# Optimization experiments

Measured on AMD Instinct MI355X. Metric: run time of the kernel, lower is better.

## Reference

```python
import jax, jax.numpy as jnp
from jax import lax
import numpy as np


def setup_inputs() -> dict:
    key = jax.random.key(0)
    kb, ks = jax.random.split(key)
    boxes = jax.random.uniform(kb, (4, 2048, 4), dtype=jnp.float32)
    scores = jax.random.normal(ks, (4, 16, 2048), dtype=jnp.float32)
    return {
        "boxes": boxes,
        "scores": scores,
        "max_output_boxes_per_class": 100,
        "iou_threshold": jnp.float32(0.5),
        "score_threshold": jnp.float32(0.0),
    }


def _fix_boxes(boxes):
    # center_point_box == 0 path: reorder corners so x1<=x2, y1<=y2
    # (swap-if-greater in the original is equivalent to per-axis min/max)
    x1, y1, x2, y2 = boxes[..., 0], boxes[..., 1], boxes[..., 2], boxes[..., 3]
    return jnp.stack(
        [jnp.minimum(x1, x2), jnp.minimum(y1, y2), jnp.maximum(x1, x2), jnp.maximum(y1, y2)],
        axis=-1,
    )


def _nms_single(boxes, scores, iou_thr, score_thr, K):
    # boxes: [N,4] (xyxy, already fixed), scores: [N]
    N = boxes.shape[0]
    order = jnp.argsort(-scores)  # stable sort -> ties broken by index, like torchvision
    b = boxes[order]
    x1, y1, x2, y2 = b[:, 0], b[:, 1], b[:, 2], b[:, 3]
    area = (x2 - x1) * (y2 - y1)
    idxs = jnp.arange(N)

    def step(suppressed, k):
        kept = ~suppressed[k]
        ix1 = jnp.maximum(b[k, 0], x1)
        iy1 = jnp.maximum(b[k, 1], y1)
        ix2 = jnp.minimum(b[k, 2], x2)
        iy2 = jnp.minimum(b[k, 3], y2)
        inter = jnp.maximum(ix2 - ix1, 0.0) * jnp.maximum(iy2 - iy1, 0.0)
        iou = inter / (area[k] + area - inter)
        suppressed = suppressed | (kept & (iou > iou_thr) & (idxs > k))
        return suppressed, kept

    _, keep = lax.scan(step, jnp.zeros((N,), bool), idxs)  # keep: [N] in score order
    rank = jnp.cumsum(keep) - 1
    slot = jnp.where(keep & (rank < K), rank, K)  # slot K is out-of-bounds -> dropped
    sel = jnp.full((K,), -1, jnp.int32).at[slot].set(order.astype(jnp.int32), mode="drop")
    # original truncates the top-K selection to the COUNT of selected boxes passing score_thr
    sel_valid = sel >= 0
    count = jnp.sum(sel_valid & (scores[jnp.maximum(sel, 0)] >= score_thr))
    return jnp.where(jnp.arange(K) < count, sel, -1)


def reference(boxes, scores, max_output_boxes_per_class, iou_threshold, score_threshold):
    B, N, _ = boxes.shape
    C = scores.shape[1]
    K = int(max_output_boxes_per_class)
    fb = _fix_boxes(boxes)
    f = lambda bx, sc: _nms_single(bx, sc, iou_threshold, score_threshold, K)
    # vmap over classes (boxes shared), then over batch
    sel = jax.vmap(jax.vmap(f, in_axes=(None, 0)), in_axes=(0, 0))(fb, scores)  # [B,C,K]
    valid = sel >= 0
    bidx = jnp.broadcast_to(jnp.arange(B, dtype=jnp.int32)[:, None, None], sel.shape)
    cidx = jnp.broadcast_to(jnp.arange(C, dtype=jnp.int32)[None, :, None], sel.shape)
    out = jnp.stack([jnp.where(valid, bidx, -1), jnp.where(valid, cidx, -1), sel], axis=-1)
    # fixed-shape padded version of the original ragged [num_selected, 3] output;
    # invalid rows are all -1
    return out.reshape(B * C * K, 3)
```

## Files before the change

kernel.cpp:

```cpp
#include <hip/hip_runtime.h>

#define NN 2048
#define NT 256
#define NB 4
#define NC 16
#define NCLS (NB * NC)
#define CHUNKS 8
#define TILE 64
#define NTILES (NN / TILE)
#define KKEEP 176

typedef unsigned long long u64;

__device__ __forceinline__ u64 make_key(float s, int idx) {
  unsigned u = __float_as_uint(s);
  u ^= (u >> 31) ? 0xFFFFFFFFu : 0x80000000u;
  u = ~u;
  return ((u64)u << 32) | (unsigned)idx;
}
__device__ __forceinline__ float key_score(u64 key) {
  unsigned u = ~(unsigned)(key >> 32);
  unsigned bits = (u >> 31) ? (u ^ 0x80000000u) : ~u;
  return __uint_as_float(bits);
}

__device__ __forceinline__ float iou_f(float kx1, float ky1, float kx2, float ky2, float ka,
                                       float x1, float y1, float x2, float y2, float a) {
  float ix1 = fmaxf(kx1, x1);
  float iy1 = fmaxf(ky1, y1);
  float ix2 = fminf(kx2, x2);
  float iy2 = fminf(ky2, y2);
  float iw = fmaxf(ix2 - ix1, 0.0f);
  float ih = fmaxf(iy2 - iy1, 0.0f);
  float inter = iw * ih;
  asm volatile("" : "+v"(inter));
  float denom = ka + a - inter;
  return inter / denom;
}

__global__ __launch_bounds__(NT) void rank_kernel(
    const float* __restrict__ boxes,
    const float* __restrict__ scores,
    float* __restrict__ wx1, float* __restrict__ wy1,
    float* __restrict__ wx2, float* __restrict__ wy2,
    float* __restrict__ wsc, int* __restrict__ widx)
{
  __shared__ u64 s_key[NN];

  const int blk   = blockIdx.x;
  const int bc    = blk >> 3;
  const int chunk = blk & 7;
  const int b     = bc >> 4;
  const int t     = threadIdx.x;

  {
    const float4* s4 = (const float4*)(scores + (size_t)bc * NN);
    float4 v0 = s4[t * 2], v1 = s4[t * 2 + 1];
    const int g = t * 8;
    s_key[g + 0] = make_key(v0.x, g + 0);
    s_key[g + 1] = make_key(v0.y, g + 1);
    s_key[g + 2] = make_key(v0.z, g + 2);
    s_key[g + 3] = make_key(v0.w, g + 3);
    s_key[g + 4] = make_key(v1.x, g + 4);
    s_key[g + 5] = make_key(v1.y, g + 5);
    s_key[g + 6] = make_key(v1.z, g + 6);
    s_key[g + 7] = make_key(v1.w, g + 7);
  }
  __syncthreads();

  const int i = chunk * NT + t;
  const u64 my = s_key[i];

  int r0 = 0, r1 = 0, r2 = 0, r3 = 0;
#pragma unroll 4
  for (int j = 0; j < NN; j += 4) {
    r0 += (s_key[j + 0] < my) ? 1 : 0;
    r1 += (s_key[j + 1] < my) ? 1 : 0;
    r2 += (s_key[j + 2] < my) ? 1 : 0;
    r3 += (s_key[j + 3] < my) ? 1 : 0;
  }
  const int rank = r0 + r1 + r2 + r3;

  const int idx = (int)(unsigned)(my & 0xFFFFFFFFu);
  float4 v = *(const float4*)(boxes + ((size_t)b * NN + idx) * 4);
  float x1 = fminf(v.x, v.z), x2 = fmaxf(v.x, v.z);
  float y1 = fminf(v.y, v.w), y2 = fmaxf(v.y, v.w);

  const size_t o = (size_t)bc * NN + rank;
  wx1[o] = x1; wy1[o] = y1;
  wx2[o] = x2; wy2[o] = y2;
  wsc[o] = key_score(my);
  widx[o] = idx;
}

__global__ __launch_bounds__(NT) void greedy_kernel(
    const float* __restrict__ wx1, const float* __restrict__ wy1,
    const float* __restrict__ wx2, const float* __restrict__ wy2,
    const float* __restrict__ wsc, const int* __restrict__ widx,
    const float* __restrict__ iou_thr_p, const float* __restrict__ score_thr_p,
    int K, int* __restrict__ out)
{
  __shared__ float s_kx1[KKEEP], s_ky1[KKEEP], s_kx2[KKEEP], s_ky2[KKEEP], s_ka[KKEEP];
  __shared__ float s_tx1[TILE], s_ty1[TILE], s_tx2[TILE], s_ty2[TILE], s_ts[TILE];
  __shared__ int   s_tidx[TILE];
  __shared__ u64   s_colmask[4][TILE];
  __shared__ u64   s_dead[4];
  __shared__ int   s_total;

  const int bc = blockIdx.x;
  const int b  = bc >> 4;
  const int c  = bc & 15;
  const int t  = threadIdx.x;
  const int wv = t >> 6;
  const int ln = t & 63;

  const float iou_thr = *iou_thr_p;
  const float sthr    = *score_thr_p;

  int* orow = out + (size_t)bc * K * 3;
  for (int i = t; i < K * 3; i += NT) orow[i] = -1;
  if (t == 0) s_total = 0;

  const size_t base0 = (size_t)bc * NN;
  __syncthreads();

  for (int tile = 0; tile < NTILES; tile++) {
    const int base = tile * TILE;

    if      (wv == 0) { s_tx1[ln] = wx1[base0 + base + ln]; s_ts[ln]   = wsc[base0 + base + ln]; }
    else if (wv == 1) { s_ty1[ln] = wy1[base0 + base + ln]; s_tidx[ln] = widx[base0 + base + ln]; }
    else if (wv == 2) { s_tx2[ln] = wx2[base0 + base + ln]; }
    else              { s_ty2[ln] = wy2[base0 + base + ln]; }
    const int kcount = s_total;
    __syncthreads();

    float jx1 = s_tx1[ln], jy1 = s_ty1[ln], jx2 = s_tx2[ln], jy2 = s_ty2[ln];
    float ja  = (jx2 - jx1) * (jy2 - jy1);
    u64 m = 0ULL;
    for (int r = 0; r < 16; r++) {
      int il = wv * 16 + r;
      if (il < ln) {
        float rx1 = s_tx1[il], ry1 = s_ty1[il], rx2 = s_tx2[il], ry2 = s_ty2[il];
        float ra  = (rx2 - rx1) * (ry2 - ry1);
        float iou = iou_f(rx1, ry1, rx2, ry2, ra, jx1, jy1, jx2, jy2, ja);
        if (iou > iou_thr) m |= (1ULL << il);
      }
    }
    s_colmask[wv][ln] = m;

    bool dead = false;
    for (int ki = wv; ki < kcount; ki += 4) {
      float iou = iou_f(s_kx1[ki], s_ky1[ki], s_kx2[ki], s_ky2[ki], s_ka[ki],
                        jx1, jy1, jx2, jy2, ja);
      if (iou > iou_thr) { dead = true; break; }
    }
    s_dead[wv] = __ballot(dead);
    __syncthreads();

    if (t < 64) {
      u64 mc = s_colmask[0][ln] | s_colmask[1][ln] | s_colmask[2][ln] | s_colmask[3][ln];
      u64 alive = ~(s_dead[0] | s_dead[1] | s_dead[2] | s_dead[3]);
      for (int i = 0; i < TILE; i++) {
        if ((alive >> i) & 1ULL) {
          u64 kill = __ballot((int)((mc >> i) & 1ULL));
          alive &= ~kill;
        }
      }
      int total0 = s_total;
      bool kept = (alive >> ln) & 1ULL;
      int pos = __popcll(alive & ((1ULL << ln) - 1ULL));
      if (kept) {
        int kpos = total0 + pos;
        s_kx1[kpos] = jx1; s_ky1[kpos] = jy1;
        s_kx2[kpos] = jx2; s_ky2[kpos] = jy2; s_ka[kpos] = ja;
        if (kpos < K && s_ts[ln] >= sthr) {
          orow[kpos * 3 + 0] = b;
          orow[kpos * 3 + 1] = c;
          orow[kpos * 3 + 2] = s_tidx[ln];
        }
      }
      if (ln == 0) s_total = total0 + (int)__popcll(alive);
    }
    __syncthreads();
    if (s_total >= K) break;
  }
}

extern "C" void kernel_launch(void* const* d_in, const int* in_sizes, int n_in,
                              void* d_out, int out_size, void* d_ws, size_t ws_size,
                              hipStream_t stream) {
  const float* boxes  = (const float*)d_in[0];
  const float* scores = (const float*)d_in[1];
  const float* iou_p  = (const float*)d_in[3];
  const float* sth_p  = (const float*)d_in[4];
  int* out = (int*)d_out;

  const int K = out_size / (NCLS * 3);
  const size_t plane = (size_t)NCLS * NN;

  float* w   = (float*)d_ws;
  float* wx1 = w + 0 * plane;
  float* wy1 = w + 1 * plane;
  float* wx2 = w + 2 * plane;
  float* wy2 = w + 3 * plane;
  float* wsc = w + 4 * plane;
  int*  widx = (int*)(w + 5 * plane);

  hipLaunchKernelGGL(rank_kernel, dim3(NCLS * CHUNKS), dim3(NT), 0, stream,
                     boxes, scores, wx1, wy1, wx2, wy2, wsc, widx);
  hipLaunchKernelGGL(greedy_kernel, dim3(NCLS), dim3(NT), 0, stream,
                     wx1, wy1, wx2, wy2, wsc, widx, iou_p, sth_p, K, out);
}
```

Before: 53.17 us.

## Precompute sort keys in separate kernel and rank from global memory

Adds a key_kernel that writes the 64-bit score/index keys once per class to workspace. The rank kernel then reads keys straight from global memory (wave-uniform broadcast loads through the cache) instead of building a 16KB LDS copy in every block, and the rank loop is unrolled to 8 accumulators. This removes the redundant per-chunk key construction and the LDS barrier, but adds a kernel launch and swaps LDS reads for scalar or global loads whose latency may be higher.

```diff
diff --git a/kernel.cpp b/kernel.cpp
--- a/kernel.cpp
+++ b/kernel.cpp
@@ -38,48 +38,54 @@
   return inter / denom;
 }
 
+__global__ __launch_bounds__(NT) void key_kernel(
+    const float* __restrict__ scores, u64* __restrict__ keys)
+{
+  const int bc = blockIdx.x;
+  const int t  = threadIdx.x;
+  const float4* s4 = (const float4*)(scores + (size_t)bc * NN);
+  float4 v0 = s4[t * 2], v1 = s4[t * 2 + 1];
+  const int g = t * 8;
+  u64* kp = keys + (size_t)bc * NN + g;
+  kp[0] = make_key(v0.x, g + 0);
+  kp[1] = make_key(v0.y, g + 1);
+  kp[2] = make_key(v0.z, g + 2);
+  kp[3] = make_key(v0.w, g + 3);
+  kp[4] = make_key(v1.x, g + 4);
+  kp[5] = make_key(v1.y, g + 5);
+  kp[6] = make_key(v1.z, g + 6);
+  kp[7] = make_key(v1.w, g + 7);
+}
+
 __global__ __launch_bounds__(NT) void rank_kernel(
+    const u64* __restrict__ keys,
     const float* __restrict__ boxes,
-    const float* __restrict__ scores,
     float* __restrict__ wx1, float* __restrict__ wy1,
     float* __restrict__ wx2, float* __restrict__ wy2,
     float* __restrict__ wsc, int* __restrict__ widx)
 {
-  __shared__ u64 s_key[NN];
-
   const int blk   = blockIdx.x;
   const int bc    = blk >> 3;
   const int chunk = blk & 7;
   const int b     = bc >> 4;
   const int t     = threadIdx.x;
 
-  {
-    const float4* s4 = (const float4*)(scores + (size_t)bc * NN);
-    float4 v0 = s4[t * 2], v1 = s4[t * 2 + 1];
-    const int g = t * 8;
-    s_key[g + 0] = make_key(v0.x, g + 0);
-    s_key[g + 1] = make_key(v0.y, g + 1);
-    s_key[g + 2] = make_key(v0.z, g + 2);
-    s_key[g + 3] = make_key(v0.w, g + 3);
-    s_key[g + 4] = make_key(v1.x, g + 4);
-    s_key[g + 5] = make_key(v1.y, g + 5);
-    s_key[g + 6] = make_key(v1.z, g + 6);
-    s_key[g + 7] = make_key(v1.w, g + 7);
+  const u64* __restrict__ kcls = keys + (size_t)bc * NN;
+  const int i = chunk * NT + t;
+  const u64 my = kcls[i];
+
+  int r0 = 0, r1 = 0, r2 = 0, r3 = 0, r4 = 0, r5 = 0, r6 = 0, r7 = 0;
+  for (int j = 0; j < NN; j += 8) {
+    r0 += (kcls[j + 0] < my) ? 1 : 0;
+    r1 += (kcls[j + 1] < my) ? 1 : 0;
+    r2 += (kcls[j + 2] < my) ? 1 : 0;
+    r3 += (kcls[j + 3] < my) ? 1 : 0;
+    r4 += (kcls[j + 4] < my) ? 1 : 0;
+    r5 += (kcls[j + 5] < my) ? 1 : 0;
+    r6 += (kcls[j + 6] < my) ? 1 : 0;
+    r7 += (kcls[j + 7] < my) ? 1 : 0;
   }
-  __syncthreads();
-
-  const int i = chunk * NT + t;
-  const u64 my = s_key[i];
-
-  int r0 = 0, r1 = 0, r2 = 0, r3 = 0;
-#pragma unroll 4
-  for (int j = 0; j < NN; j += 4) {
-    r0 += (s_key[j + 0] < my) ? 1 : 0;
-    r1 += (s_key[j + 1] < my) ? 1 : 0;
-    r2 += (s_key[j + 2] < my) ? 1 : 0;
-    r3 += (s_key[j + 3] < my) ? 1 : 0;
-  }
-  const int rank = r0 + r1 + r2 + r3;
+  const int rank = ((r0 + r1) + (r2 + r3)) + ((r4 + r5) + (r6 + r7));
 
   const int idx = (int)(unsigned)(my & 0xFFFFFFFFu);
   float4 v = *(const float4*)(boxes + ((size_t)b * NN + idx) * 4);
@@ -205,9 +211,11 @@
   float* wy2 = w + 3 * plane;
   float* wsc = w + 4 * plane;
   int*  widx = (int*)(w + 5 * plane);
-
+  u64*  keys = (u64*)(w + 6 * plane);
+
+  hipLaunchKernelGGL(key_kernel, dim3(NCLS), dim3(NT), 0, stream, scores, keys);
   hipLaunchKernelGGL(rank_kernel, dim3(NCLS * CHUNKS), dim3(NT), 0, stream,
-                     boxes, scores, wx1, wy1, wx2, wy2, wsc, widx);
+                     keys, boxes, wx1, wy1, wx2, wy2, wsc, widx);
   hipLaunchKernelGGL(greedy_kernel, dim3(NCLS), dim3(NT), 0, stream,
                      wx1, wy1, wx2, wy2, wsc, widx, iou_p, sth_p, K, out);
 }
```

Measured after the change: 76.90 us. 1.45x slower.

## Rank scores via register-held keys and readlane broadcasts instead of LDS scans

Applied to the files above, without the earlier changes.

The rank kernel stops staging all 2048 keys in shared memory. Each lane now keeps 32 score keys in registers and broadcasts them to the wavefront with v_readlane, while every thread ranks two elements, so the grid drops from 512 to 256 blocks. This removes the LDS reads and the block barrier from the rank step. In exchange it adds scalar readlane traffic and higher register pressure, and it halves the number of blocks.

```diff
diff --git a/kernel.cpp b/kernel.cpp
--- a/kernel.cpp
+++ b/kernel.cpp
@@ -5,23 +5,19 @@
 #define NB 4
 #define NC 16
 #define NCLS (NB * NC)
-#define CHUNKS 8
 #define TILE 64
 #define NTILES (NN / TILE)
 #define KKEEP 176
 
 typedef unsigned long long u64;
 
-__device__ __forceinline__ u64 make_key(float s, int idx) {
+__device__ __forceinline__ unsigned score_hi(float s) {
   unsigned u = __float_as_uint(s);
   u ^= (u >> 31) ? 0xFFFFFFFFu : 0x80000000u;
-  u = ~u;
-  return ((u64)u << 32) | (unsigned)idx;
-}
-__device__ __forceinline__ float key_score(u64 key) {
-  unsigned u = ~(unsigned)(key >> 32);
-  unsigned bits = (u >> 31) ? (u ^ 0x80000000u) : ~u;
-  return __uint_as_float(bits);
+  return ~u;
+}
+__device__ __forceinline__ u64 make_key(float s, int idx) {
+  return ((u64)score_hi(s) << 32) | (unsigned)idx;
 }
 
 __device__ __forceinline__ float iou_f(float kx1, float ky1, float kx2, float ky2, float ka,
@@ -39,58 +35,65 @@
 }
 
 __global__ __launch_bounds__(NT) void rank_kernel(
+    const float* __restrict__ scores,
     const float* __restrict__ boxes,
-    const float* __restrict__ scores,
     float* __restrict__ wx1, float* __restrict__ wy1,
     float* __restrict__ wx2, float* __restrict__ wy2,
     float* __restrict__ wsc, int* __restrict__ widx)
 {
-  __shared__ u64 s_key[NN];
-
-  const int blk   = blockIdx.x;
-  const int bc    = blk >> 3;
-  const int chunk = blk & 7;
-  const int b     = bc >> 4;
-  const int t     = threadIdx.x;
-
+  const int blk = blockIdx.x;
+  const int bc  = blk >> 2;
+  const int q   = blk & 3;
+  const int b   = bc >> 4;
+  const int t   = threadIdx.x;
+  const int ln  = t & 63;
+
+  const float* __restrict__ scls = scores + (size_t)bc * NN;
+
+  unsigned hi[32];
+#pragma unroll
+  for (int r = 0; r < 32; r++) hi[r] = score_hi(scls[r * 64 + ln]);
+
+  const int i0 = q * 512 + t;
+  const int i1 = i0 + 256;
+  const float sc0 = scls[i0];
+  const float sc1 = scls[i1];
+  const u64 my0 = make_key(sc0, i0);
+  const u64 my1 = make_key(sc1, i1);
+
+  int ra0 = 0, rb0 = 0, ra1 = 0, rb1 = 0;
+#pragma unroll
+  for (int r = 0; r < 32; r++) {
+#pragma unroll 8
+    for (int l = 0; l < 64; l++) {
+      unsigned khi;
+      asm("v_readlane_b32 %0, %1, %2" : "=s"(khi) : "v"(hi[r]), "s"(l));
+      u64 kj = ((u64)khi << 32) | (unsigned)(r * 64 + l);
+      if (l & 1) { rb0 += (kj < my0) ? 1 : 0; rb1 += (kj < my1) ? 1 : 0; }
+      else       { ra0 += (kj < my0) ? 1 : 0; ra1 += (kj < my1) ? 1 : 0; }
+    }
+  }
+  const int rank0 = ra0 + rb0;
+  const int rank1 = ra1 + rb1;
+
+  const float* __restrict__ bbase = boxes + (size_t)b * NN * 4;
+  const size_t obase = (size_t)bc * NN;
   {
-    const float4* s4 = (const float4*)(scores + (size_t)bc * NN);
-    float4 v0 = s4[t * 2], v1 = s4[t * 2 + 1];
-    const int g = t * 8;
-    s_key[g + 0] = make_key(v0.x, g + 0);
-    s_key[g + 1] = make_key(v0.y, g + 1);
-    s_key[g + 2] = make_key(v0.z, g + 2);
-    s_key[g + 3] = make_key(v0.w, g + 3);
-    s_key[g + 4] = make_key(v1.x, g + 4);
-    s_key[g + 5] = make_key(v1.y, g + 5);
-    s_key[g + 6] = make_key(v1.z, g + 6);
-    s_key[g + 7] = make_key(v1.w, g + 7);
-  }
-  __syncthreads();
-
-  const int i = chunk * NT + t;
-  const u64 my = s_key[i];
-
-  int r0 = 0, r1 = 0, r2 = 0, r3 = 0;
-#pragma unroll 4
-  for (int j = 0; j < NN; j += 4) {
-    r0 += (s_key[j + 0] < my) ? 1 : 0;
-    r1 += (s_key[j + 1] < my) ? 1 : 0;
-    r2 += (s_key[j + 2] < my) ? 1 : 0;
-    r3 += (s_key[j + 3] < my) ? 1 : 0;
-  }
-  const int rank = r0 + r1 + r2 + r3;
-
-  const int idx = (int)(unsigned)(my & 0xFFFFFFFFu);
-  float4 v = *(const float4*)(boxes + ((size_t)b * NN + idx) * 4);
-  float x1 = fminf(v.x, v.z), x2 = fmaxf(v.x, v.z);
-  float y1 = fminf(v.y, v.w), y2 = fmaxf(v.y, v.w);
-
-  const size_t o = (size_t)bc * NN + rank;
-  wx1[o] = x1; wy1[o] = y1;
-  wx2[o] = x2; wy2[o] = y2;
-  wsc[o] = key_score(my);
-  widx[o] = idx;
+    float4 v = *(const float4*)(bbase + (size_t)i0 * 4);
+    float x1 = fminf(v.x, v.z), x2 = fmaxf(v.x, v.z);
+    float y1 = fminf(v.y, v.w), y2 = fmaxf(v.y, v.w);
+    const size_t o = obase + rank0;
+    wx1[o] = x1; wy1[o] = y1; wx2[o] = x2; wy2[o] = y2;
+    wsc[o] = sc0; widx[o] = i0;
+  }
+  {
+    float4 v = *(const float4*)(bbase + (size_t)i1 * 4);
+    float x1 = fminf(v.x, v.z), x2 = fmaxf(v.x, v.z);
+    float y1 = fminf(v.y, v.w), y2 = fmaxf(v.y, v.w);
+    const size_t o = obase + rank1;
+    wx1[o] = x1; wy1[o] = y1; wx2[o] = x2; wy2[o] = y2;
+    wsc[o] = sc1; widx[o] = i1;
+  }
 }
 
 __global__ __launch_bounds__(NT) void greedy_kernel(
@@ -206,8 +209,8 @@
   float* wsc = w + 4 * plane;
   int*  widx = (int*)(w + 5 * plane);
 
-  hipLaunchKernelGGL(rank_kernel, dim3(NCLS * CHUNKS), dim3(NT), 0, stream,
-                     boxes, scores, wx1, wy1, wx2, wy2, wsc, widx);
+  hipLaunchKernelGGL(rank_kernel, dim3(NCLS * 4), dim3(NT), 0, stream,
+                     scores, boxes, wx1, wy1, wx2, wy2, wsc, widx);
   hipLaunchKernelGGL(greedy_kernel, dim3(NCLS), dim3(NT), 0, stream,
                      wx1, wy1, wx2, wy2, wsc, widx, iou_p, sth_p, K, out);
 }
```

Result: slower. 113.7 us (+113.8%).
